# Kernel tuning notes

Measured on AMD Instinct MI355X. Metric: run time of the kernel, lower is better.

## Reference

```python
import jax, jax.numpy as jnp
import numpy as np

EPS = 1e-5
GROUPS = 32


def setup_inputs() -> dict:
    key = jax.random.key(0)
    ks = jax.random.split(key, 12)
    b, c, h, w = 8, 256, 64, 64
    s = 1.0 / np.sqrt(c)
    return {
        "x": jax.random.normal(ks[0], (b, c, h, w), jnp.float32),
        "gn_w": jax.random.uniform(ks[1], (c,), jnp.float32, 0.5, 1.5),
        "gn_b": jax.random.normal(ks[2], (c,), jnp.float32) * 0.1,
        "wq": jax.random.normal(ks[3], (c, c), jnp.float32) * s,
        "bq": jax.random.normal(ks[4], (c,), jnp.float32) * 0.02,
        "wk": jax.random.normal(ks[5], (c, c), jnp.float32) * s,
        "bk": jax.random.normal(ks[6], (c,), jnp.float32) * 0.02,
        "wv": jax.random.normal(ks[7], (c, c), jnp.float32) * s,
        "bv": jax.random.normal(ks[8], (c,), jnp.float32) * 0.02,
        "wp": jax.random.normal(ks[9], (c, c), jnp.float32) * s,
        "bp": jax.random.normal(ks[10], (c,), jnp.float32) * 0.02,
        "gamma": jax.random.normal(ks[11], (1,), jnp.float32),
    }


def _group_norm(x, weight, bias):
    b, c, h, w = x.shape
    g = min(c, GROUPS)
    xg = x.reshape(b, g, c // g, h * w)
    mean = xg.mean(axis=(2, 3), keepdims=True)
    var = jnp.var(xg, axis=(2, 3), keepdims=True)
    xn = (xg - mean) * jax.lax.rsqrt(var + EPS)
    xn = xn.reshape(b, c, h, w)
    return xn * weight[None, :, None, None] + bias[None, :, None, None]


def reference(x, gn_w, gn_b, wq, bq, wk, bk, wv, bv, wp, bp, gamma):
    b, c, h, w = x.shape
    x_dash = _group_norm(x, gn_w, gn_b)           # (b,c,h,w)
    xf = x_dash.reshape(b, c, h * w)              # (b,c,n)
    # 1x1 convs == per-pixel linear maps over channels
    q = jnp.einsum('oc,bcn->bon', wq, xf) + bq[None, :, None]
    k = jnp.einsum('oc,bcn->bon', wk, xf) + bk[None, :, None]
    v = jnp.einsum('oc,bcn->bon', wv, xf) + bv[None, :, None]
    # attn[b,i,j] = <q[:,i], k[:,j]> / sqrt(c)
    attn = jnp.einsum('bci,bcj->bij', q, k) / jnp.sqrt(jnp.asarray(c, x.dtype))
    attn = jax.nn.softmax(attn, axis=-1)
    # out[b,c,i] = sum_j v[b,c,j] * attn[b,i,j]
    out = jnp.einsum('bcj,bij->bci', v, attn)
    out = jnp.einsum('oc,bcn->bon', wp, out) + bp[None, :, None]
    out = out.reshape(b, c, h, w)
    return x + gamma[0] * out
```

## Files before the change

kernel.cpp:

```cpp
#include <hip/hip_runtime.h>
#include <cstdint>
#include <cstddef>


#define NB   8
#define NC   256
#define NPIX 4096
#define CPG  8

typedef __attribute__((ext_vector_type(8))) short bf16x8;
typedef __attribute__((ext_vector_type(4))) short s16x4;
typedef __attribute__((ext_vector_type(8))) short s16x8;
typedef __attribute__((ext_vector_type(4))) float f32x4;

__device__ __forceinline__ short f2bf(float f) {
  union { float f; uint32_t u; } v; v.f = f;
  return (short)((v.u + 0x7fffu + ((v.u >> 16) & 1u)) >> 16);
}

__device__ __forceinline__ uint32_t cvtpk_bf(float a, float b) {
  uint32_t r;
  asm("v_cvt_pk_bf16_f32 %0, %1, %2" : "=v"(r) : "v"(a), "v"(b));
  return r;
}

__device__ __forceinline__ f32x4 mfma16(bf16x8 a, bf16x8 b, f32x4 c) {
  return __builtin_amdgcn_mfma_f32_16x16x32_bf16(a, b, c, 0, 0, 0);
}

__device__ __forceinline__ void gload_lds16(const short* g, short* l) {
  __builtin_amdgcn_global_load_lds(
      (const __attribute__((address_space(1))) void*)g,
      (__attribute__((address_space(3))) void*)l, 16, 0, 0);
}

__global__ __launch_bounds__(256) void wconv4(
    const float* __restrict__ w0, const float* __restrict__ w1,
    const float* __restrict__ w2, const float* __restrict__ w3,
    short* __restrict__ o0, short* __restrict__ o1,
    short* __restrict__ o2, short* __restrict__ o3) {
  int m = blockIdx.x >> 6;
  const float* w = (m == 0) ? w0 : (m == 1) ? w1 : (m == 2) ? w2 : w3;
  short* o = (m == 0) ? o0 : (m == 1) ? o1 : (m == 2) ? o2 : o3;
  int i = ((blockIdx.x & 63) * 256 + threadIdx.x) * 4;
  float4 v = *reinterpret_cast<const float4*>(w + i);
  s16x4 p;
  p[0] = f2bf(v.x); p[1] = f2bf(v.y); p[2] = f2bf(v.z); p[3] = f2bf(v.w);
  *reinterpret_cast<s16x4*>(o + i) = p;
}

__global__ __launch_bounds__(256) void gnorm(const float* __restrict__ x,
                                             const float* __restrict__ gw,
                                             const float* __restrict__ gb,
                                             short* __restrict__ xdt) {
  int b = blockIdx.x >> 5;
  int g = blockIdx.x & 31;
  const float* xp = x + ((size_t)b * NC + (size_t)g * CPG) * NPIX;
  int t = threadIdx.x;

  float s = 0.f, ss = 0.f;
  const float4* xp4 = reinterpret_cast<const float4*>(xp);
  for (int i = t; i < (CPG * NPIX) / 4; i += 256) {
    float4 v = xp4[i];
    s  += v.x + v.y + v.z + v.w;
    ss += v.x * v.x + v.y * v.y + v.z * v.z + v.w * v.w;
  }
  for (int m = 32; m; m >>= 1) { s += __shfl_xor(s, m); ss += __shfl_xor(ss, m); }
  __shared__ float red[10];
  int wid = t >> 6;
  if ((t & 63) == 0) { red[wid] = s; red[4 + wid] = ss; }
  __syncthreads();
  if (t == 0) {
    float a  = red[0] + red[1] + red[2] + red[3];
    float b2 = red[4] + red[5] + red[6] + red[7];
    float mean = a * (1.f / 32768.f);
    float var  = b2 * (1.f / 32768.f) - mean * mean;
    red[8] = mean;
    red[9] = rsqrtf(var + 1e-5f);
  }
  __syncthreads();
  float mean = red[8], rstd = red[9];

  float wv2[CPG], bv2[CPG];
  for (int cc = 0; cc < CPG; ++cc) {
    float wgt = gw[g * CPG + cc] * rstd;
    wv2[cc] = wgt;
    bv2[cc] = gb[g * CPG + cc] - mean * wgt;
  }
  for (int pix = t; pix < NPIX; pix += 256) {
    s16x8 pk;
    for (int cc = 0; cc < CPG; ++cc)
      pk[cc] = f2bf(fmaf(xp[cc * NPIX + pix], wv2[cc], bv2[cc]));
    *reinterpret_cast<s16x8*>(&xdt[((size_t)b * NPIX + pix) * NC + g * CPG]) = pk;
  }
}

__global__ __launch_bounds__(256) void qkv_gemm(
    const short* __restrict__ wq_bf, const short* __restrict__ wk_bf,
    const short* __restrict__ wv_bf,
    const float* __restrict__ bq, const float* __restrict__ bk,
    const float* __restrict__ bv,
    const short* __restrict__ xdt,
    short* __restrict__ qt, short* __restrict__ kt, short* __restrict__ vv) {
  int nt = blockIdx.x, b = blockIdx.y, mi = blockIdx.z;
  const short* W; const float* bia;
  if (mi == 0)      { W = wq_bf; bia = bq; }
  else if (mi == 1) { W = wk_bf; bia = bk; }
  else              { W = wv_bf; bia = bv; }

  __shared__ short xtile[64 * 256];
  __shared__ float bias_lds[256];
  int t = threadIdx.x;
  const short* xg = xdt + ((size_t)b * NPIX + nt * 64) * NC;
  for (int it = 0; it < 8; ++it) {
    int id = t + it * 256, row = id >> 5, part = id & 31;
    *reinterpret_cast<uint4*>(&xtile[row * 256 + (part ^ (row & 7)) * 8]) =
        *reinterpret_cast<const uint4*>(&xg[(size_t)row * 256 + part * 8]);
  }
  bias_lds[t] = bia[t];
  __syncthreads();

  int w = t >> 6, lane = t & 63, g = lane >> 4, lr = lane & 15;
  f32x4 acc[4][4];
  f32x4 zz = {0.f, 0.f, 0.f, 0.f};
  for (int i = 0; i < 4; ++i) for (int j = 0; j < 4; ++j) acc[i][j] = zz;

  for (int c0 = 0; c0 < 256; c0 += 32) {
    bf16x8 af[4], bfr[4];
    for (int mf = 0; mf < 4; ++mf)
      af[mf] = *reinterpret_cast<const bf16x8*>(
          &W[(size_t)(w * 64 + mf * 16 + lr) * 256 + c0 + g * 8]);
    for (int nf = 0; nf < 4; ++nf) {
      int row = nf * 16 + lr;
      bfr[nf] = *reinterpret_cast<const bf16x8*>(
          &xtile[row * 256 + (((c0 >> 3) + g) ^ (row & 7)) * 8]);
    }
    for (int mf = 0; mf < 4; ++mf)
      for (int nf = 0; nf < 4; ++nf)
        acc[mf][nf] = mfma16(af[mf], bfr[nf], acc[mf][nf]);
  }

  if (mi < 2) {
    short* outp = (mi == 0) ? qt : kt;
    for (int mf = 0; mf < 4; ++mf)
      for (int nf = 0; nf < 4; ++nf) {
        int ob = w * 64 + mf * 16 + g * 4;
        int n  = nt * 64 + nf * 16 + lr;
        s16x4 pk;
        for (int r = 0; r < 4; ++r)
          pk[r] = f2bf(acc[mf][nf][r] + bias_lds[ob + r]);
        *reinterpret_cast<s16x4*>(&outp[((size_t)b * NPIX + n) * NC + ob]) = pk;
      }
  } else {
    for (int mf = 0; mf < 4; ++mf)
      for (int nf = 0; nf < 4; ++nf) {
        int ob = w * 64 + mf * 16 + g * 4;
        int n  = nt * 64 + nf * 16 + lr;
        for (int r = 0; r < 4; ++r)
          vv[((size_t)b * NC + ob + r) * NPIX + n] =
              f2bf(acc[mf][nf][r] + bias_lds[ob + r]);
      }
  }
}

__global__ __launch_bounds__(256, 2) void attn(
    const short* __restrict__ qt, const short* __restrict__ kt,
    const short* __restrict__ vv, short* __restrict__ ot) {
  int b = blockIdx.x, itile = blockIdx.y;
  __shared__ short ktile[64 * 256];
  __shared__ short Pb[2][64 * 64];
  __shared__ float alpha_lds[2][64];

  int t = threadIdx.x, w = t >> 6, lane = t & 63, g = lane >> 4, lr = lane & 15;
  int i0 = itile * 64;

  const short* ktg = kt + (size_t)b * NPIX * NC;

  for (int it = 0; it < 8; ++it) {
    int id = it * 256 + t, row = id >> 5, ch = id & 31;
    gload_lds16(ktg + row * 256 + (ch ^ (row & 7)) * 8, &ktile[id * 8]);
  }
  const short* kgp = ktg + 16384;

  bf16x8 qf[8];
  {
    const short* qrow = qt + ((size_t)b * NPIX + i0 + w * 16 + lr) * NC;
    for (int ks = 0; ks < 8; ++ks)
      qf[ks] = *reinterpret_cast<const bf16x8*>(&qrow[ks * 32 + g * 8]);
  }

  const short* vp = vv + (size_t)b * NC * NPIX + (size_t)(w * 64 + lr) * NPIX + g * 8;

  int q_loc = w * 16 + lr;
  int pw[4];
  for (int mf = 0; mf < 4; ++mf)
    pw[mf] = q_loc * 64 + (((mf * 2 + (g >> 1)) ^ (q_loc & 7)) * 8) + (g & 1) * 4;
  int pr[4][2];
  for (int nf = 0; nf < 4; ++nf)
    for (int ks2 = 0; ks2 < 2; ++ks2) {
      int qq = nf * 16 + lr;
      pr[nf][ks2] = qq * 64 + (((ks2 * 4 + g) ^ (qq & 7)) * 8);
    }

  f32x4 zz = {0.f, 0.f, 0.f, 0.f};
  f32x4 oacc[4][4];
  for (int i = 0; i < 4; ++i) for (int j = 0; j < 4; ++j) oacc[i][j] = zz;
  bf16x8 va[2][4];
  float m_ = -1e30f, l_ = 0.f;

  const float sc = 0.0625f, L2E = 1.44269504f;
  const float SCL = sc * L2E;

  for (int jt = 0; jt < 64; ++jt) {
    int cur = jt & 1, prv = cur ^ 1;

    asm volatile("s_waitcnt vmcnt(0) lgkmcnt(0)" ::: "memory");
    __builtin_amdgcn_s_barrier();
    asm volatile("" ::: "memory");

    if (jt > 0) {
      float av[4];
      for (int nf = 0; nf < 4; ++nf) av[nf] = alpha_lds[prv][nf * 16 + lr];
      if (__any((av[0] != 1.f) | (av[1] != 1.f) | (av[2] != 1.f) | (av[3] != 1.f))) {
        for (int mf = 0; mf < 4; ++mf)
          for (int nf = 0; nf < 4; ++nf) oacc[mf][nf] *= av[nf];
      }
      __builtin_amdgcn_s_setprio(1);
      for (int ks2 = 0; ks2 < 2; ++ks2) {
        bf16x8 pb[4];
        for (int nf = 0; nf < 4; ++nf)
          pb[nf] = *reinterpret_cast<const bf16x8*>(&Pb[prv][pr[nf][ks2]]);
        for (int mf = 0; mf < 4; ++mf)
          for (int nf = 0; nf < 4; ++nf)
            oacc[mf][nf] = mfma16(va[ks2][mf], pb[nf], oacc[mf][nf]);
      }
      __builtin_amdgcn_s_setprio(0);
    }

    for (int ks2 = 0; ks2 < 2; ++ks2)
      for (int mf = 0; mf < 4; ++mf)
        va[ks2][mf] = *reinterpret_cast<const bf16x8*>(
            vp + (size_t)mf * (16 * NPIX) + ks2 * 32);
    vp += 64;

    f32x4 s[4];
    for (int mf = 0; mf < 4; ++mf) s[mf] = zz;
    __builtin_amdgcn_s_setprio(1);
    for (int ks = 0; ks < 8; ++ks) {
      bf16x8 kf[4];
      for (int mf = 0; mf < 4; ++mf) {
        int row = mf * 16 + lr;
        kf[mf] = *reinterpret_cast<const bf16x8*>(
            &ktile[row * 256 + (((ks * 4) + g) ^ (row & 7)) * 8]);
      }
      for (int mf = 0; mf < 4; ++mf) s[mf] = mfma16(kf[mf], qf[ks], s[mf]);
    }
    __builtin_amdgcn_s_setprio(0);

    asm volatile("s_waitcnt lgkmcnt(0)" ::: "memory");
    __builtin_amdgcn_s_barrier();
    asm volatile("" ::: "memory");

    for (int it = 0; it < 8; ++it) {
      int id = it * 256 + t, row = id >> 5, ch = id & 31;
      gload_lds16(kgp + row * 256 + (ch ^ (row & 7)) * 8, &ktile[id * 8]);
    }
    kgp += 16384;

    float mx = s[0][0];
    for (int mf = 0; mf < 4; ++mf)
      for (int r = 0; r < 4; ++r) mx = fmaxf(mx, s[mf][r]);
    mx = fmaxf(mx, __shfl_xor(mx, 16));
    mx = fmaxf(mx, __shfl_xor(mx, 32));
    float pm = mx * sc;
    float mn = (pm - m_ <= 8.f) ? m_ : pm;
    float alpha = exp2f((m_ - mn) * L2E);
    float mnl = mn * L2E;
    float ps = 0.f;
    for (int mf = 0; mf < 4; ++mf) {
      float p0 = exp2f(fmaf(s[mf][0], SCL, -mnl));
      float p1 = exp2f(fmaf(s[mf][1], SCL, -mnl));
      float p2 = exp2f(fmaf(s[mf][2], SCL, -mnl));
      float p3 = exp2f(fmaf(s[mf][3], SCL, -mnl));
      ps += p0 + p1 + p2 + p3;
      uint2 pk;
      pk.x = cvtpk_bf(p0, p1);
      pk.y = cvtpk_bf(p2, p3);
      *reinterpret_cast<uint2*>(&Pb[cur][pw[mf]]) = pk;
    }
    ps += __shfl_xor(ps, 16);
    ps += __shfl_xor(ps, 32);
    l_ = l_ * alpha + ps;
    m_ = mn;
    if (lane < 16) alpha_lds[cur][w * 16 + lane] = alpha;
  }

  asm volatile("s_waitcnt vmcnt(0) lgkmcnt(0)" ::: "memory");
  __builtin_amdgcn_s_barrier();
  asm volatile("" ::: "memory");
  {
    float av[4];
    for (int nf = 0; nf < 4; ++nf) av[nf] = alpha_lds[1][nf * 16 + lr];
    if (__any((av[0] != 1.f) | (av[1] != 1.f) | (av[2] != 1.f) | (av[3] != 1.f))) {
      for (int mf = 0; mf < 4; ++mf)
        for (int nf = 0; nf < 4; ++nf) oacc[mf][nf] *= av[nf];
    }
    for (int ks2 = 0; ks2 < 2; ++ks2) {
      bf16x8 pb[4];
      for (int nf = 0; nf < 4; ++nf)
        pb[nf] = *reinterpret_cast<const bf16x8*>(&Pb[1][pr[nf][ks2]]);
      for (int mf = 0; mf < 4; ++mf)
        for (int nf = 0; nf < 4; ++nf)
          oacc[mf][nf] = mfma16(va[ks2][mf], pb[nf], oacc[mf][nf]);
    }
  }

  if (lane < 16) alpha_lds[0][w * 16 + lane] = l_;
  __syncthreads();

  for (int nf = 0; nf < 4; ++nf) {
    float inv = 1.f / alpha_lds[0][nf * 16 + lr];
    int i = i0 + nf * 16 + lr;
    for (int mf = 0; mf < 4; ++mf) {
      int cb = w * 64 + mf * 16 + g * 4;
      s16x4 pk;
      for (int r = 0; r < 4; ++r) pk[r] = f2bf(oacc[mf][nf][r] * inv);
      *reinterpret_cast<s16x4*>(&ot[((size_t)b * NPIX + i) * NC + cb]) = pk;
    }
  }
}

__global__ __launch_bounds__(256) void proj_res(
    const short* __restrict__ wp_bf, const float* __restrict__ bp,
    const short* __restrict__ ot, const float* __restrict__ x,
    const float* __restrict__ gamma, float* __restrict__ out) {
  int nt = blockIdx.x, b = blockIdx.y;
  __shared__ short otile[64 * 256];
  __shared__ float bias_lds[256];
  int t = threadIdx.x;
  const short* og = ot + ((size_t)b * NPIX + nt * 64) * NC;
  for (int itx = 0; itx < 8; ++itx) {
    int id = t + itx * 256, row = id >> 5, part = id & 31;
    *reinterpret_cast<uint4*>(&otile[row * 256 + (part ^ (row & 7)) * 8]) =
        *reinterpret_cast<const uint4*>(&og[(size_t)row * 256 + part * 8]);
  }
  bias_lds[t] = bp[t];
  __syncthreads();

  int w = t >> 6, lane = t & 63, g = lane >> 4, lr = lane & 15;
  f32x4 acc[4][4];
  f32x4 zz = {0.f, 0.f, 0.f, 0.f};
  for (int i = 0; i < 4; ++i) for (int j = 0; j < 4; ++j) acc[i][j] = zz;

  for (int c0 = 0; c0 < 256; c0 += 32) {
    bf16x8 af[4], bfr[4];
    for (int mf = 0; mf < 4; ++mf)
      af[mf] = *reinterpret_cast<const bf16x8*>(
          &wp_bf[(size_t)(w * 64 + mf * 16 + lr) * 256 + c0 + g * 8]);
    for (int nf = 0; nf < 4; ++nf) {
      int row = nf * 16 + lr;
      bfr[nf] = *reinterpret_cast<const bf16x8*>(
          &otile[row * 256 + (((c0 >> 3) + g) ^ (row & 7)) * 8]);
    }
    for (int mf = 0; mf < 4; ++mf)
      for (int nf = 0; nf < 4; ++nf)
        acc[mf][nf] = mfma16(af[mf], bfr[nf], acc[mf][nf]);
  }

  float gm = gamma[0];
  for (int mf = 0; mf < 4; ++mf)
    for (int nf = 0; nf < 4; ++nf) {
      int ob = w * 64 + mf * 16 + g * 4;
      int n  = nt * 64 + nf * 16 + lr;
      for (int r = 0; r < 4; ++r) {
        size_t idx = ((size_t)b * NC + ob + r) * NPIX + n;
        out[idx] = x[idx] + gm * (acc[mf][nf][r] + bias_lds[ob + r]);
      }
    }
}

extern "C" void kernel_launch(void* const* d_in, const int* in_sizes, int n_in,
                              void* d_out, int out_size, void* d_ws, size_t ws_size,
                              hipStream_t stream) {
  (void)in_sizes; (void)n_in; (void)out_size; (void)ws_size;
  const float* x     = (const float*)d_in[0];
  const float* gn_w  = (const float*)d_in[1];
  const float* gn_b  = (const float*)d_in[2];
  const float* wq    = (const float*)d_in[3];
  const float* bq    = (const float*)d_in[4];
  const float* wk    = (const float*)d_in[5];
  const float* bk    = (const float*)d_in[6];
  const float* wv    = (const float*)d_in[7];
  const float* bv    = (const float*)d_in[8];
  const float* wp    = (const float*)d_in[9];
  const float* bp    = (const float*)d_in[10];
  const float* gamma = (const float*)d_in[11];
  float* out = (float*)d_out;

  char* ws = (char*)d_ws;
  const size_t WSZ = 131072;
  const size_t TSZ = (size_t)NB * NPIX * NC * 2;
  short* wq_bf = (short*)(ws);
  short* wk_bf = (short*)(ws + WSZ);
  short* wv_bf = (short*)(ws + 2 * WSZ);
  short* wp_bf = (short*)(ws + 3 * WSZ);
  short* xdt   = (short*)(ws + 4 * WSZ);
  short* qt    = (short*)(ws + 4 * WSZ + TSZ);
  short* kt    = (short*)(ws + 4 * WSZ + 2 * TSZ);
  short* vv    = (short*)(ws + 4 * WSZ + 3 * TSZ);
  short* ot    = xdt;

  wconv4<<<256, 256, 0, stream>>>(wq, wk, wv, wp, wq_bf, wk_bf, wv_bf, wp_bf);

  gnorm<<<256, 256, 0, stream>>>(x, gn_w, gn_b, xdt);

  qkv_gemm<<<dim3(64, 8, 3), 256, 0, stream>>>(wq_bf, wk_bf, wv_bf, bq, bk, bv,
                                               xdt, qt, kt, vv);

  attn<<<dim3(8, 64), 256, 0, stream>>>(qt, kt, vv, ot);

  proj_res<<<dim3(64, 8), 256, 0, stream>>>(wp_bf, bp, ot, x, gamma, out);
}
```

Before: 307.1 us.

## Reuse x tile across Q/K/V in one block and retile attention QK^T as 2x2 warps

The QKV GEMM now loads each x tile into LDS once and loops over the three weight matrices inside the block, so the grid z dimension of three goes away and the x tile is read once instead of three times. In attention, the four warps now split the QK^T product 2x2 over key and query halves. Each warp loads two K fragments instead of four and reuses each across two query fragments. The row max and row sum are combined across the paired warps through a small LDS exchange. This trades fewer LDS K reads for extra Q registers, an extra cross-warp exchange, and a third as many GEMM blocks, which lowers parallelism in that kernel.

```diff
diff --git a/kernel.cpp b/kernel.cpp
--- a/kernel.cpp
+++ b/kernel.cpp
@@ -102,14 +102,10 @@
     const float* __restrict__ bv,
     const short* __restrict__ xdt,
     short* __restrict__ qt, short* __restrict__ kt, short* __restrict__ vv) {
-  int nt = blockIdx.x, b = blockIdx.y, mi = blockIdx.z;
-  const short* W; const float* bia;
-  if (mi == 0)      { W = wq_bf; bia = bq; }
-  else if (mi == 1) { W = wk_bf; bia = bk; }
-  else              { W = wv_bf; bia = bv; }
+  int nt = blockIdx.x, b = blockIdx.y;
 
   __shared__ short xtile[64 * 256];
-  __shared__ float bias_lds[256];
+  __shared__ float bias_lds[3][256];
   int t = threadIdx.x;
   const short* xg = xdt + ((size_t)b * NPIX + nt * 64) * NC;
   for (int it = 0; it < 8; ++it) {
@@ -117,49 +113,56 @@
     *reinterpret_cast<uint4*>(&xtile[row * 256 + (part ^ (row & 7)) * 8]) =
         *reinterpret_cast<const uint4*>(&xg[(size_t)row * 256 + part * 8]);
   }
-  bias_lds[t] = bia[t];
+  bias_lds[0][t] = bq[t];
+  bias_lds[1][t] = bk[t];
+  bias_lds[2][t] = bv[t];
   __syncthreads();
 
   int w = t >> 6, lane = t & 63, g = lane >> 4, lr = lane & 15;
-  f32x4 acc[4][4];
-  f32x4 zz = {0.f, 0.f, 0.f, 0.f};
-  for (int i = 0; i < 4; ++i) for (int j = 0; j < 4; ++j) acc[i][j] = zz;
-
-  for (int c0 = 0; c0 < 256; c0 += 32) {
-    bf16x8 af[4], bfr[4];
-    for (int mf = 0; mf < 4; ++mf)
-      af[mf] = *reinterpret_cast<const bf16x8*>(
-          &W[(size_t)(w * 64 + mf * 16 + lr) * 256 + c0 + g * 8]);
-    for (int nf = 0; nf < 4; ++nf) {
-      int row = nf * 16 + lr;
-      bfr[nf] = *reinterpret_cast<const bf16x8*>(
-          &xtile[row * 256 + (((c0 >> 3) + g) ^ (row & 7)) * 8]);
-    }
-    for (int mf = 0; mf < 4; ++mf)
-      for (int nf = 0; nf < 4; ++nf)
-        acc[mf][nf] = mfma16(af[mf], bfr[nf], acc[mf][nf]);
-  }
-
-  if (mi < 2) {
-    short* outp = (mi == 0) ? qt : kt;
-    for (int mf = 0; mf < 4; ++mf)
+  const short* Ws[3] = {wq_bf, wk_bf, wv_bf};
+
+  for (int mi = 0; mi < 3; ++mi) {
+    const short* W = Ws[mi];
+    f32x4 acc[4][4];
+    f32x4 zz = {0.f, 0.f, 0.f, 0.f};
+    for (int i = 0; i < 4; ++i) for (int j = 0; j < 4; ++j) acc[i][j] = zz;
+
+    for (int c0 = 0; c0 < 256; c0 += 32) {
+      bf16x8 af[4], bfr[4];
+      for (int mf = 0; mf < 4; ++mf)
+        af[mf] = *reinterpret_cast<const bf16x8*>(
+            &W[(size_t)(w * 64 + mf * 16 + lr) * 256 + c0 + g * 8]);
       for (int nf = 0; nf < 4; ++nf) {
-        int ob = w * 64 + mf * 16 + g * 4;
-        int n  = nt * 64 + nf * 16 + lr;
-        s16x4 pk;
-        for (int r = 0; r < 4; ++r)
-          pk[r] = f2bf(acc[mf][nf][r] + bias_lds[ob + r]);
-        *reinterpret_cast<s16x4*>(&outp[((size_t)b * NPIX + n) * NC + ob]) = pk;
+        int row = nf * 16 + lr;
+        bfr[nf] = *reinterpret_cast<const bf16x8*>(
+            &xtile[row * 256 + (((c0 >> 3) + g) ^ (row & 7)) * 8]);
       }
-  } else {
-    for (int mf = 0; mf < 4; ++mf)
-      for (int nf = 0; nf < 4; ++nf) {
-        int ob = w * 64 + mf * 16 + g * 4;
-        int n  = nt * 64 + nf * 16 + lr;
-        for (int r = 0; r < 4; ++r)
-          vv[((size_t)b * NC + ob + r) * NPIX + n] =
-              f2bf(acc[mf][nf][r] + bias_lds[ob + r]);
-      }
+      for (int mf = 0; mf < 4; ++mf)
+        for (int nf = 0; nf < 4; ++nf)
+          acc[mf][nf] = mfma16(af[mf], bfr[nf], acc[mf][nf]);
+    }
+
+    if (mi < 2) {
+      short* outp = (mi == 0) ? qt : kt;
+      for (int mf = 0; mf < 4; ++mf)
+        for (int nf = 0; nf < 4; ++nf) {
+          int ob = w * 64 + mf * 16 + g * 4;
+          int n  = nt * 64 + nf * 16 + lr;
+          s16x4 pk;
+          for (int r = 0; r < 4; ++r)
+            pk[r] = f2bf(acc[mf][nf][r] + bias_lds[mi][ob + r]);
+          *reinterpret_cast<s16x4*>(&outp[((size_t)b * NPIX + n) * NC + ob]) = pk;
+        }
+    } else {
+      for (int mf = 0; mf < 4; ++mf)
+        for (int nf = 0; nf < 4; ++nf) {
+          int ob = w * 64 + mf * 16 + g * 4;
+          int n  = nt * 64 + nf * 16 + lr;
+          for (int r = 0; r < 4; ++r)
+            vv[((size_t)b * NC + ob + r) * NPIX + n] =
+                f2bf(acc[mf][nf][r] + bias_lds[2][ob + r]);
+        }
+    }
   }
 }
 
@@ -170,8 +173,10 @@
   __shared__ short ktile[64 * 256];
   __shared__ short Pb[2][64 * 64];
   __shared__ float alpha_lds[2][64];
+  __shared__ float exch[2][64];
 
   int t = threadIdx.x, w = t >> 6, lane = t & 63, g = lane >> 4, lr = lane & 15;
+  int kk = w >> 1, qq = w & 1;
   int i0 = itile * 64;
 
   const short* ktg = kt + (size_t)b * NPIX * NC;
@@ -182,31 +187,38 @@
   }
   const short* kgp = ktg + 16384;
 
-  bf16x8 qf[8];
-  {
-    const short* qrow = qt + ((size_t)b * NPIX + i0 + w * 16 + lr) * NC;
+  bf16x8 qf[2][8];
+  for (int qi = 0; qi < 2; ++qi) {
+    const short* qrow =
+        qt + ((size_t)b * NPIX + i0 + 32 * qq + 16 * qi + lr) * NC;
     for (int ks = 0; ks < 8; ++ks)
-      qf[ks] = *reinterpret_cast<const bf16x8*>(&qrow[ks * 32 + g * 8]);
+      qf[qi][ks] = *reinterpret_cast<const bf16x8*>(&qrow[ks * 32 + g * 8]);
   }
 
   const short* vp = vv + (size_t)b * NC * NPIX + (size_t)(w * 64 + lr) * NPIX + g * 8;
 
-  int q_loc = w * 16 + lr;
-  int pw[4];
-  for (int mf = 0; mf < 4; ++mf)
-    pw[mf] = q_loc * 64 + (((mf * 2 + (g >> 1)) ^ (q_loc & 7)) * 8) + (g & 1) * 4;
+  int row0 = 32 * kk + lr, row1 = row0 + 16;
+  int eidx[2], pwo[2][2];
+  for (int qi = 0; qi < 2; ++qi) {
+    int q_loc = 32 * qq + 16 * qi + lr;
+    eidx[qi] = q_loc;
+    for (int mt = 0; mt < 2; ++mt)
+      pwo[qi][mt] = q_loc * 64 +
+                    (((4 * kk + 2 * mt + (g >> 1)) ^ (q_loc & 7)) * 8) +
+                    (g & 1) * 4;
+  }
   int pr[4][2];
   for (int nf = 0; nf < 4; ++nf)
     for (int ks2 = 0; ks2 < 2; ++ks2) {
-      int qq = nf * 16 + lr;
-      pr[nf][ks2] = qq * 64 + (((ks2 * 4 + g) ^ (qq & 7)) * 8);
+      int qc = nf * 16 + lr;
+      pr[nf][ks2] = qc * 64 + (((ks2 * 4 + g) ^ (qc & 7)) * 8);
     }
 
   f32x4 zz = {0.f, 0.f, 0.f, 0.f};
   f32x4 oacc[4][4];
   for (int i = 0; i < 4; ++i) for (int j = 0; j < 4; ++j) oacc[i][j] = zz;
   bf16x8 va[2][4];
-  float m_ = -1e30f, l_ = 0.f;
+  float m_[2] = {-1e30f, -1e30f}, l_p[2] = {0.f, 0.f};
 
   const float sc = 0.0625f, L2E = 1.44269504f;
   const float SCL = sc * L2E;
@@ -243,19 +255,36 @@
             vp + (size_t)mf * (16 * NPIX) + ks2 * 32);
     vp += 64;
 
-    f32x4 s[4];
-    for (int mf = 0; mf < 4; ++mf) s[mf] = zz;
+    f32x4 s[2][2];
+    s[0][0] = zz; s[0][1] = zz; s[1][0] = zz; s[1][1] = zz;
     __builtin_amdgcn_s_setprio(1);
     for (int ks = 0; ks < 8; ++ks) {
-      bf16x8 kf[4];
-      for (int mf = 0; mf < 4; ++mf) {
-        int row = mf * 16 + lr;
-        kf[mf] = *reinterpret_cast<const bf16x8*>(
-            &ktile[row * 256 + (((ks * 4) + g) ^ (row & 7)) * 8]);
-      }
-      for (int mf = 0; mf < 4; ++mf) s[mf] = mfma16(kf[mf], qf[ks], s[mf]);
+      bf16x8 kf0 = *reinterpret_cast<const bf16x8*>(
+          &ktile[row0 * 256 + (((ks * 4) + g) ^ (row0 & 7)) * 8]);
+      bf16x8 kf1 = *reinterpret_cast<const bf16x8*>(
+          &ktile[row1 * 256 + (((ks * 4) + g) ^ (row1 & 7)) * 8]);
+      s[0][0] = mfma16(kf0, qf[0][ks], s[0][0]);
+      s[0][1] = mfma16(kf0, qf[1][ks], s[0][1]);
+      s[1][0] = mfma16(kf1, qf[0][ks], s[1][0]);
+      s[1][1] = mfma16(kf1, qf[1][ks], s[1][1]);
     }
     __builtin_amdgcn_s_setprio(0);
+
+    float mx[2];
+    for (int qi = 0; qi < 2; ++qi) {
+      float m0 = fmaxf(fmaxf(s[0][qi][0], s[0][qi][1]),
+                       fmaxf(s[0][qi][2], s[0][qi][3]));
+      float m1 = fmaxf(fmaxf(s[1][qi][0], s[1][qi][1]),
+                       fmaxf(s[1][qi][2], s[1][qi][3]));
+      float m = fmaxf(m0, m1);
+      m = fmaxf(m, __shfl_xor(m, 16));
+      m = fmaxf(m, __shfl_xor(m, 32));
+      mx[qi] = m;
+    }
+    if (lane < 16) {
+      exch[kk][32 * qq + lr]      = mx[0];
+      exch[kk][32 * qq + 16 + lr] = mx[1];
+    }
 
     asm volatile("s_waitcnt lgkmcnt(0)" ::: "memory");
     __builtin_amdgcn_s_barrier();
@@ -267,32 +296,27 @@
     }
     kgp += 16384;
 
-    float mx = s[0][0];
-    for (int mf = 0; mf < 4; ++mf)
-      for (int r = 0; r < 4; ++r) mx = fmaxf(mx, s[mf][r]);
-    mx = fmaxf(mx, __shfl_xor(mx, 16));
-    mx = fmaxf(mx, __shfl_xor(mx, 32));
-    float pm = mx * sc;
-    float mn = (pm - m_ <= 8.f) ? m_ : pm;
-    float alpha = exp2f((m_ - mn) * L2E);
-    float mnl = mn * L2E;
-    float ps = 0.f;
-    for (int mf = 0; mf < 4; ++mf) {
-      float p0 = exp2f(fmaf(s[mf][0], SCL, -mnl));
-      float p1 = exp2f(fmaf(s[mf][1], SCL, -mnl));
-      float p2 = exp2f(fmaf(s[mf][2], SCL, -mnl));
-      float p3 = exp2f(fmaf(s[mf][3], SCL, -mnl));
-      ps += p0 + p1 + p2 + p3;
-      uint2 pk;
-      pk.x = cvtpk_bf(p0, p1);
-      pk.y = cvtpk_bf(p2, p3);
-      *reinterpret_cast<uint2*>(&Pb[cur][pw[mf]]) = pk;
-    }
-    ps += __shfl_xor(ps, 16);
-    ps += __shfl_xor(ps, 32);
-    l_ = l_ * alpha + ps;
-    m_ = mn;
-    if (lane < 16) alpha_lds[cur][w * 16 + lane] = alpha;
+    for (int qi = 0; qi < 2; ++qi) {
+      float pm = fmaxf(mx[qi], exch[kk ^ 1][eidx[qi]]) * sc;
+      float mn = (pm - m_[qi] <= 8.f) ? m_[qi] : pm;
+      float alpha = exp2f((m_[qi] - mn) * L2E);
+      float mnl = mn * L2E;
+      float ps = 0.f;
+      for (int mt = 0; mt < 2; ++mt) {
+        float p0 = exp2f(fmaf(s[mt][qi][0], SCL, -mnl));
+        float p1 = exp2f(fmaf(s[mt][qi][1], SCL, -mnl));
+        float p2 = exp2f(fmaf(s[mt][qi][2], SCL, -mnl));
+        float p3 = exp2f(fmaf(s[mt][qi][3], SCL, -mnl));
+        ps += p0 + p1 + p2 + p3;
+        uint2 pk;
+        pk.x = cvtpk_bf(p0, p1);
+        pk.y = cvtpk_bf(p2, p3);
+        *reinterpret_cast<uint2*>(&Pb[cur][pwo[qi][mt]]) = pk;
+      }
+      l_p[qi] = l_p[qi] * alpha + ps;
+      m_[qi] = mn;
+      if (kk == 0 && lane < 16) alpha_lds[cur][eidx[qi]] = alpha;
+    }
   }
 
   asm volatile("s_waitcnt vmcnt(0) lgkmcnt(0)" ::: "memory");
@@ -315,12 +339,22 @@
     }
   }
 
-  if (lane < 16) alpha_lds[0][w * 16 + lane] = l_;
+  for (int qi = 0; qi < 2; ++qi) {
+    float v = l_p[qi];
+    v += __shfl_xor(v, 16);
+    v += __shfl_xor(v, 32);
+    l_p[qi] = v;
+  }
+  if (lane < 16) {
+    exch[kk][32 * qq + lr]      = l_p[0];
+    exch[kk][32 * qq + 16 + lr] = l_p[1];
+  }
   __syncthreads();
 
   for (int nf = 0; nf < 4; ++nf) {
-    float inv = 1.f / alpha_lds[0][nf * 16 + lr];
-    int i = i0 + nf * 16 + lr;
+    int q = nf * 16 + lr;
+    float inv = 1.f / (exch[0][q] + exch[1][q]);
+    int i = i0 + q;
     for (int mf = 0; mf < 4; ++mf) {
       int cb = w * 64 + mf * 16 + g * 4;
       s16x4 pk;
@@ -414,8 +448,8 @@
 
   gnorm<<<256, 256, 0, stream>>>(x, gn_w, gn_b, xdt);
 
-  qkv_gemm<<<dim3(64, 8, 3), 256, 0, stream>>>(wq_bf, wk_bf, wv_bf, bq, bk, bv,
-                                               xdt, qt, kt, vv);
+  qkv_gemm<<<dim3(64, 8), 256, 0, stream>>>(wq_bf, wk_bf, wv_bf, bq, bk, bv,
+                                            xdt, qt, kt, vv);
 
   attn<<<dim3(8, 64), 256, 0, stream>>>(qt, kt, vv, ot);
 
```

New measurement: 316.8 us. 3.2% more time.
